# Optimization experiments

Measured on AMD Instinct MI355X. Metric: run time of the kernel, lower is better.

## Reference

```python
import jax, jax.numpy as jnp
import numpy as np

EPS = 1e-8

def setup_inputs() -> dict:
    key = jax.random.key(0)
    k1, k2 = jax.random.split(key)
    B, D, H, W, K = 32, 256, 64, 64, 64
    X = jax.random.normal(k1, (B, D, H, W), dtype=jnp.float32)
    std1 = 1.0 / float(np.sqrt(K * D))
    codewords = jax.random.uniform(k2, (K, D), dtype=jnp.float32, minval=-std1, maxval=std1)
    return {"X": X, "codewords": codewords}

def reference(X, codewords):
    B, D = X.shape[0], X.shape[1]
    # (B, D, H, W) -> (B, N, D)
    Xf = X.reshape(B, D, -1).transpose(0, 2, 1)
    # pairwise cosine similarity: normalize then matmul -> (B, N, K)
    Xn = Xf / jnp.maximum(jnp.linalg.norm(Xf, axis=-1, keepdims=True), EPS)
    Cn = codewords / jnp.maximum(jnp.linalg.norm(codewords, axis=-1, keepdims=True), EPS)
    L = jnp.einsum('bnd,kd->bnk', Xn, Cn)
    A = jax.nn.softmax(L, axis=2)
    # aggregate: E[b,k,d] = sum_n A[b,n,k] * (Xf[b,n,d] - C[k,d])
    # expressed without materializing the (B,N,K,D) residual tensor:
    E = jnp.einsum('bnk,bnd->bkd', A, Xf) - A.sum(axis=1)[:, :, None] * codewords[None, :, :]
    return E
```

## Files before the change

### kernel.cpp

```cpp
#include <hip/hip_runtime.h>
#include <hip/hip_bf16.h>
#include <math.h>

#define BB 32
#define DD 256
#define NN 4096
#define KK 64
#define EPSV 1e-8f
#define XSTR 264

typedef __attribute__((ext_vector_type(8))) short short8;
typedef __attribute__((ext_vector_type(4))) float f32x4;

__device__ __forceinline__ unsigned int bf16pair(float a, float b) {
    __hip_bfloat162 h = __float22bfloat162_rn(make_float2(a, b));
    return *(unsigned int*)&h;
}
__device__ __forceinline__ unsigned short bf16one(float a) {
    unsigned int ua = __float_as_uint(a);
    ua += 0x7fffu + ((ua >> 16) & 1u);
    return (unsigned short)(ua >> 16);
}

__global__ __launch_bounds__(256, 2) void k_fused(const float* __restrict__ X,
                                                  const float* __restrict__ C,
                                                  float* __restrict__ P,
                                                  float* __restrict__ Sp) {
    __shared__ unsigned short xnd_s[64 * XSTR];
    __shared__ unsigned short xdn_s[DD * 64];
    __shared__ unsigned short at_s[KK * 72];
    __shared__ float rn4[4 * 64];
    __shared__ float red_s[4 * 64];

    int t = threadIdx.x;
    int b = blockIdx.x >> 4, chunk = blockIdx.x & 15;
    int w = t >> 6, lane = t & 63, c = lane & 15, g = lane >> 4;
    int q = t >> 4;
    int n4 = c * 4;

    const float* Xb = X + (size_t)b * DD * NN + chunk * 256;

    float4 pre[16];
#pragma unroll
    for (int i = 0; i < 4; i++) {
        const float* xb = Xb + (size_t)(q * 4 + 64 * i) * NN + n4;
#pragma unroll
        for (int j = 0; j < 4; j++) pre[i * 4 + j] = *(const float4*)(xb + (size_t)j * NN);
    }

    short8 cnf[8];
    {
        int k = 16 * w + c;
        const float* cp = C + k * DD;
        float4 v0[8], v1[8];
        float ss = 0.f;
#pragma unroll
        for (int ks = 0; ks < 8; ks++) {
            v0[ks] = *(const float4*)(cp + 32 * ks + 8 * g);
            v1[ks] = *(const float4*)(cp + 32 * ks + 8 * g + 4);
            ss = fmaf(v0[ks].x, v0[ks].x, ss); ss = fmaf(v0[ks].y, v0[ks].y, ss);
            ss = fmaf(v0[ks].z, v0[ks].z, ss); ss = fmaf(v0[ks].w, v0[ks].w, ss);
            ss = fmaf(v1[ks].x, v1[ks].x, ss); ss = fmaf(v1[ks].y, v1[ks].y, ss);
            ss = fmaf(v1[ks].z, v1[ks].z, ss); ss = fmaf(v1[ks].w, v1[ks].w, ss);
        }
        ss += __shfl_xor(ss, 16);
        ss += __shfl_xor(ss, 32);
        float r = 1.f / fmaxf(sqrtf(ss), EPSV);
#pragma unroll
        for (int ks = 0; ks < 8; ks++) {
            uint4 u;
            u.x = bf16pair(v0[ks].x * r, v0[ks].y * r);
            u.y = bf16pair(v0[ks].z * r, v0[ks].w * r);
            u.z = bf16pair(v1[ks].x * r, v1[ks].y * r);
            u.w = bf16pair(v1[ks].z * r, v1[ks].w * r);
            cnf[ks] = *(short8*)&u;
        }
    }

    f32x4 eacc[4][4];
#pragma unroll
    for (int dt = 0; dt < 4; dt++)
#pragma unroll
        for (int kt = 0; kt < 4; kt++) eacc[dt][kt] = (f32x4){0.f, 0.f, 0.f, 0.f};
    float s_acc[4] = {0.f, 0.f, 0.f, 0.f};

    for (int p = 0; p < 4; p++) {
        __syncthreads();

        f32x4 ssn = (f32x4){0.f, 0.f, 0.f, 0.f};
#pragma unroll
        for (int i = 0; i < 4; i++) {
            int dbase = q * 4 + 64 * i;
            float4 r0 = pre[i * 4 + 0], r1 = pre[i * 4 + 1];
            float4 r2 = pre[i * 4 + 2], r3 = pre[i * 4 + 3];
            ssn.x = fmaf(r0.x, r0.x, ssn.x); ssn.x = fmaf(r1.x, r1.x, ssn.x);
            ssn.x = fmaf(r2.x, r2.x, ssn.x); ssn.x = fmaf(r3.x, r3.x, ssn.x);
            ssn.y = fmaf(r0.y, r0.y, ssn.y); ssn.y = fmaf(r1.y, r1.y, ssn.y);
            ssn.y = fmaf(r2.y, r2.y, ssn.y); ssn.y = fmaf(r3.y, r3.y, ssn.y);
            ssn.z = fmaf(r0.z, r0.z, ssn.z); ssn.z = fmaf(r1.z, r1.z, ssn.z);
            ssn.z = fmaf(r2.z, r2.z, ssn.z); ssn.z = fmaf(r3.z, r3.z, ssn.z);
            ssn.w = fmaf(r0.w, r0.w, ssn.w); ssn.w = fmaf(r1.w, r1.w, ssn.w);
            ssn.w = fmaf(r2.w, r2.w, ssn.w); ssn.w = fmaf(r3.w, r3.w, ssn.w);
            const float4 rr[4] = {r0, r1, r2, r3};
#pragma unroll
            for (int j = 0; j < 4; j++) {
                int d = dbase + j;
                uint2 u;
                u.x = bf16pair(rr[j].x, rr[j].y);
                u.y = bf16pair(rr[j].z, rr[j].w);
                int off = d * 64 + ((((n4 >> 3) ^ (d & 7)) << 3) | (n4 & 7));
                *(uint2*)(xdn_s + off) = u;
            }
            {
                float col[4][4] = {{r0.x, r1.x, r2.x, r3.x},
                                   {r0.y, r1.y, r2.y, r3.y},
                                   {r0.z, r1.z, r2.z, r3.z},
                                   {r0.w, r1.w, r2.w, r3.w}};
#pragma unroll
                for (int j = 0; j < 4; j++) {
                    int n = n4 + j;
                    uint2 u;
                    u.x = bf16pair(col[j][0], col[j][1]);
                    u.y = bf16pair(col[j][2], col[j][3]);
                    int blk = (dbase >> 3) ^ ((n >> 2) & 3);
                    *(uint2*)(xnd_s + n * XSTR + (blk << 3) + (dbase & 7)) = u;
                }
            }
        }

        if (p < 3) {
#pragma unroll
            for (int i = 0; i < 4; i++) {
                const float* xb = Xb + (size_t)(q * 4 + 64 * i) * NN + (p + 1) * 64 + n4;
#pragma unroll
                for (int j = 0; j < 4; j++) pre[i * 4 + j] = *(const float4*)(xb + (size_t)j * NN);
            }
        }

        ssn.x += __shfl_xor(ssn.x, 16); ssn.x += __shfl_xor(ssn.x, 32);
        ssn.y += __shfl_xor(ssn.y, 16); ssn.y += __shfl_xor(ssn.y, 32);
        ssn.z += __shfl_xor(ssn.z, 16); ssn.z += __shfl_xor(ssn.z, 32);
        ssn.w += __shfl_xor(ssn.w, 16); ssn.w += __shfl_xor(ssn.w, 32);
        if (g == 0) *(f32x4*)(rn4 + w * 64 + n4) = ssn;

        __syncthreads();

        f32x4 lacc[4];
#pragma unroll
        for (int nt = 0; nt < 4; nt++) lacc[nt] = (f32x4){0.f, 0.f, 0.f, 0.f};
#pragma unroll
        for (int ks = 0; ks < 8; ks++) {
            short8 af = cnf[ks];
#pragma unroll
            for (int nt = 0; nt < 4; nt++) {
                int n = nt * 16 + c;
                short8 bf = *(const short8*)(xnd_s + n * XSTR +
                                             (((4 * ks + g) ^ ((n >> 2) & 3)) << 3));
                lacc[nt] = __builtin_amdgcn_mfma_f32_16x16x32_bf16(af, bf, lacc[nt], 0, 0, 0);
            }
        }

        float lv[4][4];
#pragma unroll
        for (int nt = 0; nt < 4; nt++) {
            int n = nt * 16 + c;
            float ssq = rn4[n] + rn4[64 + n] + rn4[128 + n] + rn4[192 + n];
            float rn = 1.f / fmaxf(sqrtf(ssq), EPSV);
            float s = 0.f;
#pragma unroll
            for (int r = 0; r < 4; r++) {
                lv[nt][r] = __expf(lacc[nt][r] * rn);
                s += lv[nt][r];
            }
            s += __shfl_xor(s, 16);
            s += __shfl_xor(s, 32);
            if (g == 0) red_s[w * 64 + n] = s;
        }
        __syncthreads();

#pragma unroll
        for (int nt = 0; nt < 4; nt++) {
            int n = nt * 16 + c;
            float denom = red_s[n] + red_s[64 + n] + red_s[128 + n] + red_s[192 + n];
            float inv = 1.f / denom;
#pragma unroll
            for (int r = 0; r < 4; r++) {
                float a = lv[nt][r] * inv;
                s_acc[r] += a;
                int k = 16 * w + 4 * g + r;
                at_s[k * 72 + ((((n >> 3) ^ (k & 7)) << 3) | (n & 7))] = bf16one(a);
            }
        }
        __syncthreads();

#pragma unroll
        for (int ks2 = 0; ks2 < 2; ks2++) {
            short8 bk[4];
#pragma unroll
            for (int kt = 0; kt < 4; kt++) {
                int k = kt * 16 + c;
                bk[kt] = *(const short8*)(at_s + k * 72 + (((4 * ks2 + g) ^ (k & 7)) << 3));
            }
#pragma unroll
            for (int dt = 0; dt < 4; dt++) {
                int d = w * 64 + dt * 16 + c;
                short8 af = *(const short8*)(xdn_s + d * 64 + (((4 * ks2 + g) ^ (d & 7)) << 3));
#pragma unroll
                for (int kt = 0; kt < 4; kt++)
                    eacc[dt][kt] =
                        __builtin_amdgcn_mfma_f32_16x16x32_bf16(af, bk[kt], eacc[dt][kt], 0, 0, 0);
            }
        }
    }

    float* Pb = P + (size_t)blockIdx.x * (DD * KK);
#pragma unroll
    for (int dt = 0; dt < 4; dt++)
#pragma unroll
        for (int kt = 0; kt < 4; kt++)
#pragma unroll
            for (int r = 0; r < 4; r++) {
                int d = w * 64 + dt * 16 + 4 * g + r;
                Pb[d * 64 + kt * 16 + c] = eacc[dt][kt][r];
            }
#pragma unroll
    for (int r = 0; r < 4; r++) {
        float v = s_acc[r];
        v += __shfl_xor(v, 1);
        v += __shfl_xor(v, 2);
        v += __shfl_xor(v, 4);
        v += __shfl_xor(v, 8);
        if (c == 0) Sp[blockIdx.x * 64 + 16 * w + 4 * g + r] = v;
    }
}

__global__ __launch_bounds__(256) void k_fin(const float* __restrict__ P,
                                             const float* __restrict__ Sp,
                                             const float* __restrict__ C,
                                             float* __restrict__ out) {
    int idx = blockIdx.x * 256 + threadIdx.x;
    int b = idx >> 14;
    int r = idx & 16383;
    int d = r >> 6;
    int k = r & 63;
    float e = 0.f, s = 0.f;
    int base = b * 16;
#pragma unroll
    for (int cc = 0; cc < 16; cc++) {
        e += P[(size_t)(base + cc) * (DD * KK) + d * 64 + k];
        s += Sp[(base + cc) * 64 + k];
    }
    out[(size_t)(b * 64 + k) * 256 + d] = e - s * C[k * 256 + d];
}

extern "C" void kernel_launch(void* const* d_in, const int* in_sizes, int n_in,
                              void* d_out, int out_size, void* d_ws, size_t ws_size,
                              hipStream_t stream) {
    const float* X = (const float*)d_in[0];
    const float* C = (const float*)d_in[1];
    float* out = (float*)d_out;
    unsigned char* ws = (unsigned char*)d_ws;

    float* Sp = (float*)ws;
    float* P = (float*)(ws + 131072);

    k_fused<<<512, 256, 0, stream>>>(X, C, P, Sp);
    k_fin<<<2048, 256, 0, stream>>>(P, Sp, C, out);
}
```

Before: 234.0 us.

## Reduce partial results with atomics into output and halve prefetch registers

Instead of writing per-chunk partial E tiles to a workspace and summing them in a finalize kernel, each block atomically adds its E tile and soft-assignment sums directly into a zeroed output and a small sum buffer. The finalize kernel then only subtracts s*C in place. The prefetch buffer is also halved: half the d-rows are prefetched one step ahead and the other half are loaded at the start of each iteration, which lowers register pressure. This removes a 32 MB workspace write and read, at the cost of two memsets, float atomic contention across 16 chunks per batch, and nondeterministic summation order.

```diff
diff --git a/kernel.cpp b/kernel.cpp
--- a/kernel.cpp
+++ b/kernel.cpp
@@ -22,10 +22,47 @@
     return (unsigned short)(ua >> 16);
 }
 
+__device__ __forceinline__ void stage_group(int dbase, int n4, const float4* rr,
+                                            unsigned short* xnd_s, unsigned short* xdn_s,
+                                            f32x4& ssn) {
+    float4 r0 = rr[0], r1 = rr[1], r2 = rr[2], r3 = rr[3];
+    ssn.x = fmaf(r0.x, r0.x, ssn.x); ssn.x = fmaf(r1.x, r1.x, ssn.x);
+    ssn.x = fmaf(r2.x, r2.x, ssn.x); ssn.x = fmaf(r3.x, r3.x, ssn.x);
+    ssn.y = fmaf(r0.y, r0.y, ssn.y); ssn.y = fmaf(r1.y, r1.y, ssn.y);
+    ssn.y = fmaf(r2.y, r2.y, ssn.y); ssn.y = fmaf(r3.y, r3.y, ssn.y);
+    ssn.z = fmaf(r0.z, r0.z, ssn.z); ssn.z = fmaf(r1.z, r1.z, ssn.z);
+    ssn.z = fmaf(r2.z, r2.z, ssn.z); ssn.z = fmaf(r3.z, r3.z, ssn.z);
+    ssn.w = fmaf(r0.w, r0.w, ssn.w); ssn.w = fmaf(r1.w, r1.w, ssn.w);
+    ssn.w = fmaf(r2.w, r2.w, ssn.w); ssn.w = fmaf(r3.w, r3.w, ssn.w);
+#pragma unroll
+    for (int j = 0; j < 4; j++) {
+        int d = dbase + j;
+        uint2 u;
+        u.x = bf16pair(rr[j].x, rr[j].y);
+        u.y = bf16pair(rr[j].z, rr[j].w);
+        *(uint2*)(xdn_s + d * 64 + ((((n4 >> 3) ^ (d & 7)) << 3) | (n4 & 7))) = u;
+    }
+    {
+        float col[4][4] = {{r0.x, r1.x, r2.x, r3.x},
+                           {r0.y, r1.y, r2.y, r3.y},
+                           {r0.z, r1.z, r2.z, r3.z},
+                           {r0.w, r1.w, r2.w, r3.w}};
+#pragma unroll
+        for (int j = 0; j < 4; j++) {
+            int n = n4 + j;
+            uint2 u;
+            u.x = bf16pair(col[j][0], col[j][1]);
+            u.y = bf16pair(col[j][2], col[j][3]);
+            int blk = (dbase >> 3) ^ ((n >> 2) & 3);
+            *(uint2*)(xnd_s + n * XSTR + (blk << 3) + (dbase & 7)) = u;
+        }
+    }
+}
+
 __global__ __launch_bounds__(256, 2) void k_fused(const float* __restrict__ X,
                                                   const float* __restrict__ C,
-                                                  float* __restrict__ P,
-                                                  float* __restrict__ Sp) {
+                                                  float* __restrict__ out,
+                                                  float* __restrict__ Sg) {
     __shared__ unsigned short xnd_s[64 * XSTR];
     __shared__ unsigned short xdn_s[DD * 64];
     __shared__ unsigned short at_s[KK * 72];
@@ -40,9 +77,9 @@
 
     const float* Xb = X + (size_t)b * DD * NN + chunk * 256;
 
-    float4 pre[16];
-#pragma unroll
-    for (int i = 0; i < 4; i++) {
+    float4 pre[8];
+#pragma unroll
+    for (int i = 0; i < 2; i++) {
         const float* xb = Xb + (size_t)(q * 4 + 64 * i) * NN + n4;
 #pragma unroll
         for (int j = 0; j < 4; j++) pre[i * 4 + j] = *(const float4*)(xb + (size_t)j * NN);
@@ -85,52 +122,26 @@
     float s_acc[4] = {0.f, 0.f, 0.f, 0.f};
 
     for (int p = 0; p < 4; p++) {
+        float4 cur[8];
+#pragma unroll
+        for (int i = 0; i < 2; i++) {
+            const float* xb = Xb + (size_t)(q * 4 + 64 * (2 + i)) * NN + p * 64 + n4;
+#pragma unroll
+            for (int j = 0; j < 4; j++) cur[i * 4 + j] = *(const float4*)(xb + (size_t)j * NN);
+        }
         __syncthreads();
 
         f32x4 ssn = (f32x4){0.f, 0.f, 0.f, 0.f};
 #pragma unroll
-        for (int i = 0; i < 4; i++) {
-            int dbase = q * 4 + 64 * i;
-            float4 r0 = pre[i * 4 + 0], r1 = pre[i * 4 + 1];
-            float4 r2 = pre[i * 4 + 2], r3 = pre[i * 4 + 3];
-            ssn.x = fmaf(r0.x, r0.x, ssn.x); ssn.x = fmaf(r1.x, r1.x, ssn.x);
-            ssn.x = fmaf(r2.x, r2.x, ssn.x); ssn.x = fmaf(r3.x, r3.x, ssn.x);
-            ssn.y = fmaf(r0.y, r0.y, ssn.y); ssn.y = fmaf(r1.y, r1.y, ssn.y);
-            ssn.y = fmaf(r2.y, r2.y, ssn.y); ssn.y = fmaf(r3.y, r3.y, ssn.y);
-            ssn.z = fmaf(r0.z, r0.z, ssn.z); ssn.z = fmaf(r1.z, r1.z, ssn.z);
-            ssn.z = fmaf(r2.z, r2.z, ssn.z); ssn.z = fmaf(r3.z, r3.z, ssn.z);
-            ssn.w = fmaf(r0.w, r0.w, ssn.w); ssn.w = fmaf(r1.w, r1.w, ssn.w);
-            ssn.w = fmaf(r2.w, r2.w, ssn.w); ssn.w = fmaf(r3.w, r3.w, ssn.w);
-            const float4 rr[4] = {r0, r1, r2, r3};
-#pragma unroll
-            for (int j = 0; j < 4; j++) {
-                int d = dbase + j;
-                uint2 u;
-                u.x = bf16pair(rr[j].x, rr[j].y);
-                u.y = bf16pair(rr[j].z, rr[j].w);
-                int off = d * 64 + ((((n4 >> 3) ^ (d & 7)) << 3) | (n4 & 7));
-                *(uint2*)(xdn_s + off) = u;
-            }
-            {
-                float col[4][4] = {{r0.x, r1.x, r2.x, r3.x},
-                                   {r0.y, r1.y, r2.y, r3.y},
-                                   {r0.z, r1.z, r2.z, r3.z},
-                                   {r0.w, r1.w, r2.w, r3.w}};
-#pragma unroll
-                for (int j = 0; j < 4; j++) {
-                    int n = n4 + j;
-                    uint2 u;
-                    u.x = bf16pair(col[j][0], col[j][1]);
-                    u.y = bf16pair(col[j][2], col[j][3]);
-                    int blk = (dbase >> 3) ^ ((n >> 2) & 3);
-                    *(uint2*)(xnd_s + n * XSTR + (blk << 3) + (dbase & 7)) = u;
-                }
-            }
-        }
+        for (int i = 0; i < 2; i++)
+            stage_group(q * 4 + 64 * i, n4, &pre[i * 4], xnd_s, xdn_s, ssn);
+#pragma unroll
+        for (int i = 0; i < 2; i++)
+            stage_group(q * 4 + 64 * (2 + i), n4, &cur[i * 4], xnd_s, xdn_s, ssn);
 
         if (p < 3) {
 #pragma unroll
-            for (int i = 0; i < 4; i++) {
+            for (int i = 0; i < 2; i++) {
                 const float* xb = Xb + (size_t)(q * 4 + 64 * i) * NN + (p + 1) * 64 + n4;
 #pragma unroll
                 for (int j = 0; j < 4; j++) pre[i * 4 + j] = *(const float4*)(xb + (size_t)j * NN);
@@ -213,16 +224,18 @@
         }
     }
 
-    float* Pb = P + (size_t)blockIdx.x * (DD * KK);
+    float* ob = out + (size_t)b * (KK * DD);
 #pragma unroll
     for (int dt = 0; dt < 4; dt++)
 #pragma unroll
-        for (int kt = 0; kt < 4; kt++)
+        for (int kt = 0; kt < 4; kt++) {
+            int k = kt * 16 + c;
 #pragma unroll
             for (int r = 0; r < 4; r++) {
                 int d = w * 64 + dt * 16 + 4 * g + r;
-                Pb[d * 64 + kt * 16 + c] = eacc[dt][kt][r];
-            }
+                atomicAdd(&ob[k * DD + d], eacc[dt][kt][r]);
+            }
+        }
 #pragma unroll
     for (int r = 0; r < 4; r++) {
         float v = s_acc[r];
@@ -230,27 +243,18 @@
         v += __shfl_xor(v, 2);
         v += __shfl_xor(v, 4);
         v += __shfl_xor(v, 8);
-        if (c == 0) Sp[blockIdx.x * 64 + 16 * w + 4 * g + r] = v;
-    }
-}
-
-__global__ __launch_bounds__(256) void k_fin(const float* __restrict__ P,
-                                             const float* __restrict__ Sp,
+        if (c == 0) atomicAdd(&Sg[b * 64 + 16 * w + 4 * g + r], v);
+    }
+}
+
+__global__ __launch_bounds__(256) void k_fin(const float* __restrict__ Sg,
                                              const float* __restrict__ C,
                                              float* __restrict__ out) {
     int idx = blockIdx.x * 256 + threadIdx.x;
+    int d = idx & 255;
+    int k = (idx >> 8) & 63;
     int b = idx >> 14;
-    int r = idx & 16383;
-    int d = r >> 6;
-    int k = r & 63;
-    float e = 0.f, s = 0.f;
-    int base = b * 16;
-#pragma unroll
-    for (int cc = 0; cc < 16; cc++) {
-        e += P[(size_t)(base + cc) * (DD * KK) + d * 64 + k];
-        s += Sp[(base + cc) * 64 + k];
-    }
-    out[(size_t)(b * 64 + k) * 256 + d] = e - s * C[k * 256 + d];
+    out[idx] -= Sg[b * 64 + k] * C[k * 256 + d];
 }
 
 extern "C" void kernel_launch(void* const* d_in, const int* in_sizes, int n_in,
@@ -259,11 +263,10 @@
     const float* X = (const float*)d_in[0];
     const float* C = (const float*)d_in[1];
     float* out = (float*)d_out;
-    unsigned char* ws = (unsigned char*)d_ws;
-
-    float* Sp = (float*)ws;
-    float* P = (float*)(ws + 131072);
-
-    k_fused<<<512, 256, 0, stream>>>(X, C, P, Sp);
-    k_fin<<<2048, 256, 0, stream>>>(P, Sp, C, out);
-}
+    float* Sg = (float*)d_ws;
+
+    hipMemsetAsync(out, 0, (size_t)out_size * sizeof(float), stream);
+    hipMemsetAsync(Sg, 0, BB * KK * sizeof(float), stream);
+    k_fused<<<512, 256, 0, stream>>>(X, C, out, Sg);
+    k_fin<<<2048, 256, 0, stream>>>(Sg, C, out);
+}
```

Measured after the change: 299.3 us. 27.9% more time.
